# Kernel optimization log

Measured on AMD Instinct MI355X. Metric: run time of the kernel, lower is better.

Reference implementation:

```python
import jax, jax.numpy as jnp
import numpy as np

N, S, E, H = 4, 2048, 1024, 16
D = E // H  # head dim = 64


def setup_inputs() -> dict:
    key = jax.random.key(0)
    ks = jax.random.split(key, 8)
    return {
        "values": jax.random.normal(ks[0], (N, S, E), dtype=jnp.float32),
        "keys": jax.random.normal(ks[1], (N, S, E), dtype=jnp.float32),
        "queries": jax.random.normal(ks[2], (N, S, E), dtype=jnp.float32),
        "mask": jnp.ones((N, 1, 1, S), dtype=jnp.int32),
        "Wv": jax.random.normal(ks[3], (D, D), dtype=jnp.float32) / np.sqrt(D),
        "Wk": jax.random.normal(ks[4], (D, D), dtype=jnp.float32) / np.sqrt(D),
        "Wq": jax.random.normal(ks[5], (D, D), dtype=jnp.float32) / np.sqrt(D),
        "W_out": jax.random.normal(ks[6], (E, E), dtype=jnp.float32) / np.sqrt(E),
        "b_out": jnp.zeros((E,), dtype=jnp.float32),
    }


def reference(values, keys, queries, mask, Wv, Wk, Wq, W_out, b_out):
    n, q_len = queries.shape[0], queries.shape[1]
    v = values.reshape(n, -1, H, D)
    k = keys.reshape(n, -1, H, D)
    q = queries.reshape(n, q_len, H, D)
    # per-head linear projections (torch Linear: x @ W.T), shared across heads
    v = jnp.einsum('nlhd,ed->nlhe', v, Wv)
    k = jnp.einsum('nlhd,ed->nlhe', k, Wk)
    q = jnp.einsum('nqhd,ed->nqhe', q, Wq)
    # full score tensor [n, h, q, k], faithful to the original einsum
    energy = jnp.einsum('nqhd,nkhd->nhqk', q, k)
    energy = jnp.where(mask == 0, jnp.float32(-1e20), energy)
    # NOTE: original scales by sqrt(embed_size), not sqrt(head_dim)
    attention = jax.nn.softmax(energy / jnp.sqrt(jnp.float32(E)), axis=3)
    out = jnp.einsum('nhql,nlhd->nqhd', attention, v).reshape(n, q_len, E)
    out = out @ W_out.T + b_out
    return out
```

## Files before the change

### kernel.cpp

```cpp
#include <hip/hip_runtime.h>
#include <stdint.h>

#define N_B 4
#define SEQ 2048
#define EMB 1024
#define NH  16
#define HD  64
#define NHT 64
#define BQ  128
#define BK  64

typedef __attribute__((ext_vector_type(8))) short bf16x8;
typedef __attribute__((ext_vector_type(4))) float f32x4;
typedef __attribute__((ext_vector_type(2))) unsigned int u32x2;

__device__ __forceinline__ short f2bf(float x) {
  unsigned u = __float_as_uint(x);
  u += 0x7fffu + ((u >> 16) & 1u);
  return (short)(u >> 16);
}

#if __has_builtin(__builtin_amdgcn_cvt_pk_bf16_f32)
typedef __attribute__((ext_vector_type(2))) __bf16 bf16v2;
__device__ __forceinline__ unsigned pkbf(float a, float b) {
  bf16v2 r = __builtin_amdgcn_cvt_pk_bf16_f32(a, b);
  union { bf16v2 v; unsigned u; } c; c.v = r; return c.u;
}
#else
__device__ __forceinline__ unsigned pkbf(float a, float b) {
  return (unsigned)(unsigned short)f2bf(a) | ((unsigned)(unsigned short)f2bf(b) << 16);
}
#endif

__device__ __forceinline__ void swap32p(unsigned a, unsigned b, unsigned& r0, unsigned& r1) {
#if __has_builtin(__builtin_amdgcn_permlane32_swap)
  u32x2 r = __builtin_amdgcn_permlane32_swap(a, b, false, false);
  r0 = r[0]; r1 = r[1];
#else
  unsigned as = (unsigned)__shfl_xor((int)a, 32, 64), bs = (unsigned)__shfl_xor((int)b, 32, 64);
  int lo = (threadIdx.x & 32) == 0;
  r0 = lo ? a : bs;
  r1 = lo ? as : b;
#endif
}
__device__ __forceinline__ void swap16p(unsigned a, unsigned b, unsigned& r0, unsigned& r1) {
#if __has_builtin(__builtin_amdgcn_permlane16_swap)
  u32x2 r = __builtin_amdgcn_permlane16_swap(a, b, false, false);
  r0 = r[0]; r1 = r[1];
#else
  unsigned as = (unsigned)__shfl_xor((int)a, 16, 64), bs = (unsigned)__shfl_xor((int)b, 16, 64);
  int ev = (threadIdx.x & 16) == 0;
  r0 = ev ? a : bs;
  r1 = ev ? as : b;
#endif
}

__device__ __forceinline__ void glds16(const short* g, short* l) {
  __builtin_amdgcn_global_load_lds(
      (const __attribute__((address_space(1))) unsigned int*)g,
      (__attribute__((address_space(3))) unsigned int*)l, 16, 0, 0);
}

__device__ __forceinline__ int swz_src(int lane) {
  return (((lane & 7) ^ ((lane >> 3) & 7)) * 8) + ((lane >> 3) * 64);
}
__device__ __forceinline__ int swz_rd(int r, int k) {
  return r * 64 + ((k ^ (r & 7)) * 8);
}

__global__ __launch_bounds__(256) void projm_kernel(
    const float* __restrict__ Xq, const float* __restrict__ Xk, const float* __restrict__ Xv,
    const float* __restrict__ Wq, const float* __restrict__ Wk, const float* __restrict__ Wv,
    short* __restrict__ Qp, short* __restrict__ Kp, short* __restrict__ Vp,
    const float* __restrict__ Wo, short* __restrict__ Wb) {
  int tid = threadIdx.x;
  int z = blockIdx.z;
  if (z == 3) {
    int flat = blockIdx.x + blockIdx.y * 16;
    int idx = (flat * 256 + tid) * 4;
    f32x4 v = *(const f32x4*)(Wo + idx);
    uint2 u; u.x = pkbf(v.x, v.y); u.y = pkbf(v.z, v.w);
    *(uint2*)(Wb + idx) = u;
    return;
  }
  const float* X = (z == 0) ? Xq : (z == 1) ? Xk : Xv;
  const float* W = (z == 0) ? Wq : (z == 1) ? Wk : Wv;
  short* out = (z == 0) ? Qp : (z == 1) ? Kp : Vp;
  int transposed = (z == 2);
  float oscale = (z == 0) ? 0.04508422f : 1.0f;

  __shared__ __attribute__((aligned(16))) short Xs[128 * 64];
  __shared__ __attribute__((aligned(16))) short Ws[64 * 64];
  int w = tid >> 6, lane = tid & 63;
  int quad = lane >> 4, l15 = lane & 15;
  int sb = blockIdx.x * 128;
  int nh = blockIdx.y;
  int n = nh >> 4, h = nh & 15;
  int r4 = tid >> 2, c0 = (tid & 3) * 16;
  int ch0 = c0 >> 3;
#pragma unroll
  for (int rr = 0; rr < 2; rr++) {
    int row = rr * 64 + r4;
    const float* gp = X + ((size_t)(n * SEQ + sb + row)) * EMB + h * HD + c0;
    f32x4 a = *(const f32x4*)gp, b = *(const f32x4*)(gp + 4);
    f32x4 c = *(const f32x4*)(gp + 8), d = *(const f32x4*)(gp + 12);
    uint4 u0, u1;
    u0.x = pkbf(a.x, a.y); u0.y = pkbf(a.z, a.w);
    u0.z = pkbf(b.x, b.y); u0.w = pkbf(b.z, b.w);
    u1.x = pkbf(c.x, c.y); u1.y = pkbf(c.z, c.w);
    u1.z = pkbf(d.x, d.y); u1.w = pkbf(d.z, d.w);
    *(uint4*)&Xs[row * 64 + ((ch0 ^ (row & 7)) * 8)] = u0;
    *(uint4*)&Xs[row * 64 + (((ch0 + 1) ^ (row & 7)) * 8)] = u1;
  }
  {
    int e = r4;
    const float* wp = W + e * HD + c0;
    f32x4 a = *(const f32x4*)wp, b = *(const f32x4*)(wp + 4);
    f32x4 c = *(const f32x4*)(wp + 8), d = *(const f32x4*)(wp + 12);
    uint4 u0, u1;
    u0.x = pkbf(a.x, a.y); u0.y = pkbf(a.z, a.w);
    u0.z = pkbf(b.x, b.y); u0.w = pkbf(b.z, b.w);
    u1.x = pkbf(c.x, c.y); u1.y = pkbf(c.z, c.w);
    u1.z = pkbf(d.x, d.y); u1.w = pkbf(d.z, d.w);
    *(uint4*)&Ws[e * 64 + ((ch0 ^ (e & 7)) * 8)] = u0;
    *(uint4*)&Ws[e * 64 + (((ch0 + 1) ^ (e & 7)) * 8)] = u1;
  }
  __syncthreads();
  f32x4 acc[2][4] = {};
#pragma unroll
  for (int ch = 0; ch < 2; ch++) {
    bf16x8 af[2], bfr[4];
#pragma unroll
    for (int mi = 0; mi < 2; mi++)
      af[mi] = *(const bf16x8*)&Xs[swz_rd(w * 32 + mi * 16 + l15, ch * 4 + quad)];
#pragma unroll
    for (int ni = 0; ni < 4; ni++)
      bfr[ni] = *(const bf16x8*)&Ws[swz_rd(ni * 16 + l15, ch * 4 + quad)];
#pragma unroll
    for (int mi = 0; mi < 2; mi++)
#pragma unroll
      for (int ni = 0; ni < 4; ni++)
        acc[mi][ni] = __builtin_amdgcn_mfma_f32_16x16x32_bf16(af[mi], bfr[ni], acc[mi][ni], 0, 0, 0);
  }
  if (!transposed) {
#pragma unroll
    for (int mi = 0; mi < 2; mi++)
#pragma unroll
      for (int ni = 0; ni < 4; ni++)
#pragma unroll
        for (int r = 0; r < 4; r++) {
          int s = sb + w * 32 + mi * 16 + quad * 4 + r;
          out[((size_t)nh * SEQ + s) * HD + ni * 16 + l15] = f2bf(acc[mi][ni][r] * oscale);
        }
  } else {
#pragma unroll
    for (int mi = 0; mi < 2; mi++)
#pragma unroll
      for (int ni = 0; ni < 4; ni++) {
        int e2 = ni * 16 + l15;
        int s0 = sb + w * 32 + mi * 16 + quad * 4;
        uint2 u;
        u.x = pkbf(acc[mi][ni][0], acc[mi][ni][1]);
        u.y = pkbf(acc[mi][ni][2], acc[mi][ni][3]);
        *(uint2*)(out + ((size_t)nh * HD + e2) * SEQ + s0) = u;
      }
  }
}

__global__ __launch_bounds__(256, 4) void attn_kernel(
    const short* __restrict__ Qg, const short* __restrict__ Kg,
    const short* __restrict__ Vg, const int* __restrict__ maskp,
    short* __restrict__ AO) {
  __shared__ __attribute__((aligned(16))) short L[16384];

  int tid = threadIdx.x;
  int w = tid >> 6, lane = tid & 63;
  int quad = lane >> 4, l15 = lane & 15;
  int nh = blockIdx.x;
  int qt0 = blockIdx.y * BQ;
  int n = nh >> 4, h = nh & 15;
  int ssrc = swz_src(lane);
  int vrow = lane >> 3;
  int vcg = (((lane & 7) ^ ((lane >> 3) & 7)) * 8);
  const int NT = SEQ / BK;

  const short* kb = Kg + (size_t)nh * SEQ * HD;
  const short* vb = Vg + (size_t)nh * HD * SEQ;

  const short* qbase = Qg + ((size_t)nh * SEQ + qt0) * HD;
#pragma unroll
  for (int i = 0; i < 4; i++) {
    int idx = (w * 4 + i) * 512;
    glds16(qbase + idx + ssrc, &L[8192 + idx]);
  }
#pragma unroll
  for (int i = 0; i < 2; i++) {
    int idx = (w * 2 + i) * 512;
    glds16(kb + idx + ssrc, &L[idx]);
    int d = (w * 2 + i) * 8 + vrow;
    glds16(vb + (size_t)d * SEQ + vcg, &L[4096 + idx]);
  }
  int mcur = maskp[n * SEQ + lane];
  __syncthreads();
  bf16x8 qf[2][2];
#pragma unroll
  for (int nt = 0; nt < 2; nt++)
#pragma unroll
    for (int ch = 0; ch < 2; ch++)
      qf[nt][ch] = *(const bf16x8*)&L[8192 + swz_rd(w * 32 + nt * 16 + l15, ch * 4 + quad)];
  __syncthreads();

  bf16x8 vone;
#pragma unroll
  for (int j = 0; j < 8; j++) vone[j] = (short)0x3F80;

  f32x4 Oacc[2][4] = {};
  f32x4 lacc[2] = {};

  for (int kt = 0; kt < NT; kt++) {
    int cur = kt & 1;
    const short* Kb = &L[cur * 8192];
    const short* Vb = &L[cur * 8192 + 4096];
    if (kt + 1 < NT) {
      size_t k0n = (size_t)(kt + 1) * BK;
      short* Kn = &L[(cur ^ 1) * 8192];
#pragma unroll
      for (int i = 0; i < 2; i++) {
        int idx = (w * 2 + i) * 512;
        glds16(kb + k0n * HD + idx + ssrc, &Kn[idx]);
        int d = (w * 2 + i) * 8 + vrow;
        glds16(vb + (size_t)d * SEQ + k0n + vcg, &Kn[4096 + idx]);
      }
    }
    int knx = (kt + 1 < NT) ? kt + 1 : kt;
    int mnxt = maskp[n * SEQ + knx * BK + lane];

    unsigned long long mb = __ballot(mcur != 0);
    bool anymask = (mb != ~0ull);

#pragma unroll
    for (int half = 0; half < 2; half++) {
      f32x4 st[2][2];
      __builtin_amdgcn_s_setprio(1);
#pragma unroll
      for (int m2 = 0; m2 < 2; m2++) {
        int mt = half * 2 + m2;
        bf16x8 kf0 = *(const bf16x8*)&Kb[swz_rd(mt * 16 + l15, quad)];
        bf16x8 kf1 = *(const bf16x8*)&Kb[swz_rd(mt * 16 + l15, 4 + quad)];
#pragma unroll
        for (int nt = 0; nt < 2; nt++) {
          f32x4 a = {0.f, 0.f, 0.f, 0.f};
          a = __builtin_amdgcn_mfma_f32_16x16x32_bf16(kf0, qf[nt][0], a, 0, 0, 0);
          a = __builtin_amdgcn_mfma_f32_16x16x32_bf16(kf1, qf[nt][1], a, 0, 0, 0);
          st[m2][nt] = a;
        }
      }
      __builtin_amdgcn_s_setprio(0);
      if (anymask) {
#pragma unroll
        for (int m2 = 0; m2 < 2; m2++)
#pragma unroll
          for (int r = 0; r < 4; r++) {
            int kk = (half * 2 + m2) * 16 + quad * 4 + r;
            if (!((mb >> kk) & 1)) { st[m2][0][r] = -1e20f; st[m2][1][r] = -1e20f; }
          }
      }
      bf16x8 pf[2];
#pragma unroll
      for (int nt = 0; nt < 2; nt++) {
        unsigned A0 = pkbf(__builtin_amdgcn_exp2f(st[0][nt][0]), __builtin_amdgcn_exp2f(st[0][nt][1]));
        unsigned A1 = pkbf(__builtin_amdgcn_exp2f(st[0][nt][2]), __builtin_amdgcn_exp2f(st[0][nt][3]));
        unsigned B0 = pkbf(__builtin_amdgcn_exp2f(st[1][nt][0]), __builtin_amdgcn_exp2f(st[1][nt][1]));
        unsigned B1 = pkbf(__builtin_amdgcn_exp2f(st[1][nt][2]), __builtin_amdgcn_exp2f(st[1][nt][3]));
        unsigned r0, r1, s0, s1, o0, o1, o2, o3;
        swap32p(A0, B0, r0, r1);
        swap16p(r0, r1, o0, o2);
        swap32p(A1, B1, s0, s1);
        swap16p(s0, s1, o1, o3);
        union { unsigned u[4]; bf16x8 v; } c;
        c.u[0] = o0; c.u[1] = o1; c.u[2] = o2; c.u[3] = o3;
        pf[nt] = c.v;
      }

      __builtin_amdgcn_s_setprio(1);
#pragma unroll
      for (int qt = 0; qt < 2; qt++)
        lacc[qt] = __builtin_amdgcn_mfma_f32_16x16x32_bf16(pf[qt], vone, lacc[qt], 0, 0, 0);
#pragma unroll
      for (int dt = 0; dt < 4; dt++) {
        bf16x8 vf = *(const bf16x8*)&Vb[swz_rd(dt * 16 + l15, half * 4 + quad)];
#pragma unroll
        for (int qt = 0; qt < 2; qt++)
          Oacc[qt][dt] = __builtin_amdgcn_mfma_f32_16x16x32_bf16(pf[qt], vf, Oacc[qt][dt], 0, 0, 0);
      }
      __builtin_amdgcn_s_setprio(0);
    }
    mcur = mnxt;
    __syncthreads();
  }
#pragma unroll
  for (int qt = 0; qt < 2; qt++)
#pragma unroll
    for (int r = 0; r < 4; r++) {
      float inv = 1.0f / lacc[qt][r];
      int qrow = qt0 + w * 32 + qt * 16 + quad * 4 + r;
      size_t rowb = ((size_t)n * SEQ + qrow) * EMB + h * HD;
#pragma unroll
      for (int dt = 0; dt < 4; dt++)
        AO[rowb + dt * 16 + l15] = f2bf(Oacc[qt][dt][r] * inv);
    }
}

__global__ __launch_bounds__(256, 2) void gemm_kernel(const short* __restrict__ A,
                                                      const short* __restrict__ B,
                                                      const float* __restrict__ bias,
                                                      float* __restrict__ C) {
  __shared__ __attribute__((aligned(16))) short As[2][128 * 64];
  __shared__ __attribute__((aligned(16))) short Bs[2][128 * 64];
  int tid = threadIdx.x;
  int w = tid >> 6, lane = tid & 63;
  int quad = lane >> 4, l15 = lane & 15;
  int m0 = blockIdx.x * 128, n0 = blockIdx.y * 128;
  int mw = (w & 1) * 64, nw = (w >> 1) * 64;
  int lrow = lane >> 3;
  int lcg = ((lane & 7) ^ ((lane >> 3) & 7)) * 8;
  f32x4 acc[4][4] = {};
#pragma unroll
  for (int i = 0; i < 4; i++) {
    int ii = w * 4 + i;
    int r = ii * 8 + lrow;
    glds16(A + (size_t)(m0 + r) * 1024 + lcg, &As[0][ii * 512]);
    glds16(B + (size_t)(n0 + r) * 1024 + lcg, &Bs[0][ii * 512]);
  }
  __syncthreads();
  for (int kt = 0; kt < 16; kt++) {
    int cur = kt & 1;
    if (kt < 15) {
      int k0n = (kt + 1) * 64;
#pragma unroll
      for (int i = 0; i < 4; i++) {
        int ii = w * 4 + i;
        int r = ii * 8 + lrow;
        glds16(A + (size_t)(m0 + r) * 1024 + k0n + lcg, &As[cur ^ 1][ii * 512]);
        glds16(B + (size_t)(n0 + r) * 1024 + k0n + lcg, &Bs[cur ^ 1][ii * 512]);
      }
    }
#pragma unroll
    for (int ch = 0; ch < 2; ch++) {
      bf16x8 af[4], bfr[4];
#pragma unroll
      for (int mi = 0; mi < 4; mi++)
        af[mi] = *(const bf16x8*)&As[cur][swz_rd(mw + mi * 16 + l15, ch * 4 + quad)];
#pragma unroll
      for (int ni = 0; ni < 4; ni++)
        bfr[ni] = *(const bf16x8*)&Bs[cur][swz_rd(nw + ni * 16 + l15, ch * 4 + quad)];
#pragma unroll
      for (int mi = 0; mi < 4; mi++)
#pragma unroll
        for (int ni = 0; ni < 4; ni++)
          acc[mi][ni] = __builtin_amdgcn_mfma_f32_16x16x32_bf16(af[mi], bfr[ni], acc[mi][ni], 0, 0, 0);
    }
    __syncthreads();
  }
#pragma unroll
  for (int ni = 0; ni < 4; ni++) {
    int col = n0 + nw + ni * 16 + l15;
    float bv = bias[col];
#pragma unroll
    for (int mi = 0; mi < 4; mi++) {
      int rb = m0 + mw + mi * 16 + quad * 4;
#pragma unroll
      for (int r = 0; r < 4; r++)
        C[(size_t)(rb + r) * 1024 + col] = acc[mi][ni][r] + bv;
    }
  }
}

extern "C" void kernel_launch(void* const* d_in, const int* in_sizes, int n_in,
                              void* d_out, int out_size, void* d_ws, size_t ws_size,
                              hipStream_t stream) {
  const float* values  = (const float*)d_in[0];
  const float* keys    = (const float*)d_in[1];
  const float* queries = (const float*)d_in[2];
  const int*   mask    = (const int*)d_in[3];
  const float* Wv = (const float*)d_in[4];
  const float* Wk = (const float*)d_in[5];
  const float* Wq = (const float*)d_in[6];
  const float* Wo = (const float*)d_in[7];
  const float* bo = (const float*)d_in[8];
  float* out = (float*)d_out;

  short* ws = (short*)d_ws;
  short* Qp = ws;
  short* Kp = Qp + (size_t)NHT * SEQ * HD;
  short* Vp = Kp + (size_t)NHT * SEQ * HD;
  short* AO = Vp + (size_t)NHT * SEQ * HD;
  short* Wb = AO + (size_t)N_B * SEQ * EMB;

  dim3 pg(SEQ / 128, NHT, 4);
  projm_kernel<<<pg, dim3(256), 0, stream>>>(queries, keys, values, Wq, Wk, Wv,
                                             Qp, Kp, Vp, Wo, Wb);
  dim3 ag(NHT, SEQ / BQ);
  attn_kernel<<<ag, dim3(256), 0, stream>>>(Qp, Kp, Vp, mask, AO);
  dim3 gg(8192 / 128, 1024 / 128);
  gemm_kernel<<<gg, dim3(256), 0, stream>>>(AO, Wb, bo, out);
}
```

Before: 265.4 us.

## Enlarge attention query tile to 256 with 8 warps and two-tile K/V stages

Raises the attention block to 512 threads covering 256 query rows, so each K/V tile staged in LDS is reused by twice as many warps. K/V staging now processes two 64-key tiles per barrier, double-buffered across 64KB of LDS, which halves the number of __syncthreads per sequence. Q fragments are loaded straight from global into registers instead of going through LDS. The cost is a larger LDS footprint and fewer blocks (512 in total on 256 CUs), which can lower occupancy and leave load imbalance.

```diff
diff --git a/kernel.cpp b/kernel.cpp
--- a/kernel.cpp
+++ b/kernel.cpp
@@ -7,7 +7,7 @@
 #define NH  16
 #define HD  64
 #define NHT 64
-#define BQ  128
+#define BQ  256
 #define BK  64
 
 typedef __attribute__((ext_vector_type(8))) short bf16x8;
@@ -167,11 +167,11 @@
   }
 }
 
-__global__ __launch_bounds__(256, 4) void attn_kernel(
+__global__ __launch_bounds__(512, 4) void attn_kernel(
     const short* __restrict__ Qg, const short* __restrict__ Kg,
     const short* __restrict__ Vg, const int* __restrict__ maskp,
     short* __restrict__ AO) {
-  __shared__ __attribute__((aligned(16))) short L[16384];
+  __shared__ __attribute__((aligned(16))) short L[32768];
 
   int tid = threadIdx.x;
   int w = tid >> 6, lane = tid & 63;
@@ -182,32 +182,31 @@
   int ssrc = swz_src(lane);
   int vrow = lane >> 3;
   int vcg = (((lane & 7) ^ ((lane >> 3) & 7)) * 8);
-  const int NT = SEQ / BK;
+  const int NS = SEQ / (2 * BK);
 
   const short* kb = Kg + (size_t)nh * SEQ * HD;
   const short* vb = Vg + (size_t)nh * HD * SEQ;
 
-  const short* qbase = Qg + ((size_t)nh * SEQ + qt0) * HD;
-#pragma unroll
-  for (int i = 0; i < 4; i++) {
-    int idx = (w * 4 + i) * 512;
-    glds16(qbase + idx + ssrc, &L[8192 + idx]);
-  }
-#pragma unroll
-  for (int i = 0; i < 2; i++) {
-    int idx = (w * 2 + i) * 512;
-    glds16(kb + idx + ssrc, &L[idx]);
-    int d = (w * 2 + i) * 8 + vrow;
-    glds16(vb + (size_t)d * SEQ + vcg, &L[4096 + idx]);
-  }
-  int mcur = maskp[n * SEQ + lane];
-  __syncthreads();
   bf16x8 qf[2][2];
-#pragma unroll
-  for (int nt = 0; nt < 2; nt++)
-#pragma unroll
-    for (int ch = 0; ch < 2; ch++)
-      qf[nt][ch] = *(const bf16x8*)&L[8192 + swz_rd(w * 32 + nt * 16 + l15, ch * 4 + quad)];
+  {
+    const short* qb = Qg + ((size_t)nh * SEQ + qt0 + w * 32) * HD;
+#pragma unroll
+    for (int nt = 0; nt < 2; nt++)
+#pragma unroll
+      for (int ch = 0; ch < 2; ch++)
+        qf[nt][ch] = *(const bf16x8*)(qb + (nt * 16 + l15) * HD + ch * 32 + quad * 8);
+  }
+
+  auto stage_tile = [&](int t, int base) {
+    glds16(kb + (size_t)t * (BK * HD) + w * 512 + ssrc, &L[base + w * 512]);
+    int d = w * 8 + vrow;
+    glds16(vb + (size_t)d * SEQ + t * BK + vcg, &L[base + 4096 + w * 512]);
+  };
+
+  stage_tile(0, 0);
+  stage_tile(1, 8192);
+  int mA = maskp[n * SEQ + lane];
+  int mB = maskp[n * SEQ + BK + lane];
   __syncthreads();
 
   bf16x8 vone;
@@ -217,85 +216,84 @@
   f32x4 Oacc[2][4] = {};
   f32x4 lacc[2] = {};
 
-  for (int kt = 0; kt < NT; kt++) {
-    int cur = kt & 1;
-    const short* Kb = &L[cur * 8192];
-    const short* Vb = &L[cur * 8192 + 4096];
-    if (kt + 1 < NT) {
-      size_t k0n = (size_t)(kt + 1) * BK;
-      short* Kn = &L[(cur ^ 1) * 8192];
-#pragma unroll
-      for (int i = 0; i < 2; i++) {
-        int idx = (w * 2 + i) * 512;
-        glds16(kb + k0n * HD + idx + ssrc, &Kn[idx]);
-        int d = (w * 2 + i) * 8 + vrow;
-        glds16(vb + (size_t)d * SEQ + k0n + vcg, &Kn[4096 + idx]);
+  for (int s = 0; s < NS; s++) {
+    int p = s & 1;
+    if (s + 1 < NS) {
+      int t0 = 2 * s + 2;
+      stage_tile(t0, (p ^ 1) * 16384);
+      stage_tile(t0 + 1, (p ^ 1) * 16384 + 8192);
+    }
+    int tn = (s + 1 < NS) ? (2 * s + 2) : 0;
+    int mAn = maskp[n * SEQ + tn * BK + lane];
+    int mBn = maskp[n * SEQ + (tn + 1) * BK + lane];
+
+#pragma unroll
+    for (int j = 0; j < 2; j++) {
+      const short* Kb = &L[p * 16384 + j * 8192];
+      const short* Vb = Kb + 4096;
+      unsigned long long mb = __ballot((j == 0 ? mA : mB) != 0);
+      bool anymask = (mb != ~0ull);
+
+#pragma unroll
+      for (int half = 0; half < 2; half++) {
+        f32x4 st[2][2];
+        __builtin_amdgcn_s_setprio(1);
+#pragma unroll
+        for (int m2 = 0; m2 < 2; m2++) {
+          int mt = half * 2 + m2;
+          bf16x8 kf0 = *(const bf16x8*)&Kb[swz_rd(mt * 16 + l15, quad)];
+          bf16x8 kf1 = *(const bf16x8*)&Kb[swz_rd(mt * 16 + l15, 4 + quad)];
+#pragma unroll
+          for (int nt = 0; nt < 2; nt++) {
+            f32x4 a = {0.f, 0.f, 0.f, 0.f};
+            a = __builtin_amdgcn_mfma_f32_16x16x32_bf16(kf0, qf[nt][0], a, 0, 0, 0);
+            a = __builtin_amdgcn_mfma_f32_16x16x32_bf16(kf1, qf[nt][1], a, 0, 0, 0);
+            st[m2][nt] = a;
+          }
+        }
+        __builtin_amdgcn_s_setprio(0);
+        if (anymask) {
+#pragma unroll
+          for (int m2 = 0; m2 < 2; m2++)
+#pragma unroll
+            for (int r = 0; r < 4; r++) {
+              int kk = (half * 2 + m2) * 16 + quad * 4 + r;
+              if (!((mb >> kk) & 1)) { st[m2][0][r] = -1e20f; st[m2][1][r] = -1e20f; }
+            }
+        }
+        bf16x8 pf[2];
+#pragma unroll
+        for (int nt = 0; nt < 2; nt++) {
+          unsigned A0 = pkbf(__builtin_amdgcn_exp2f(st[0][nt][0]), __builtin_amdgcn_exp2f(st[0][nt][1]));
+          unsigned A1 = pkbf(__builtin_amdgcn_exp2f(st[0][nt][2]), __builtin_amdgcn_exp2f(st[0][nt][3]));
+          unsigned B0 = pkbf(__builtin_amdgcn_exp2f(st[1][nt][0]), __builtin_amdgcn_exp2f(st[1][nt][1]));
+          unsigned B1 = pkbf(__builtin_amdgcn_exp2f(st[1][nt][2]), __builtin_amdgcn_exp2f(st[1][nt][3]));
+          unsigned r0, r1, s0, s1, o0, o1, o2, o3;
+          swap32p(A0, B0, r0, r1);
+          swap16p(r0, r1, o0, o2);
+          swap32p(A1, B1, s0, s1);
+          swap16p(s0, s1, o1, o3);
+          union { unsigned u[4]; bf16x8 v; } c;
+          c.u[0] = o0; c.u[1] = o1; c.u[2] = o2; c.u[3] = o3;
+          pf[nt] = c.v;
+        }
+
+        __builtin_amdgcn_s_setprio(1);
+#pragma unroll
+        for (int qt = 0; qt < 2; qt++)
+          lacc[qt] = __builtin_amdgcn_mfma_f32_16x16x32_bf16(pf[qt], vone, lacc[qt], 0, 0, 0);
+#pragma unroll
+        for (int dt = 0; dt < 4; dt++) {
+          bf16x8 vf = *(const bf16x8*)&Vb[swz_rd(dt * 16 + l15, half * 4 + quad)];
+#pragma unroll
+          for (int qt = 0; qt < 2; qt++)
+            Oacc[qt][dt] = __builtin_amdgcn_mfma_f32_16x16x32_bf16(pf[qt], vf, Oacc[qt][dt], 0, 0, 0);
+        }
+        __builtin_amdgcn_s_setprio(0);
       }
     }
-    int knx = (kt + 1 < NT) ? kt + 1 : kt;
-    int mnxt = maskp[n * SEQ + knx * BK + lane];
-
-    unsigned long long mb = __ballot(mcur != 0);
-    bool anymask = (mb != ~0ull);
-
-#pragma unroll
-    for (int half = 0; half < 2; half++) {
-      f32x4 st[2][2];
-      __builtin_amdgcn_s_setprio(1);
-#pragma unroll
-      for (int m2 = 0; m2 < 2; m2++) {
-        int mt = half * 2 + m2;
-        bf16x8 kf0 = *(const bf16x8*)&Kb[swz_rd(mt * 16 + l15, quad)];
-        bf16x8 kf1 = *(const bf16x8*)&Kb[swz_rd(mt * 16 + l15, 4 + quad)];
-#pragma unroll
-        for (int nt = 0; nt < 2; nt++) {
-          f32x4 a = {0.f, 0.f, 0.f, 0.f};
-          a = __builtin_amdgcn_mfma_f32_16x16x32_bf16(kf0, qf[nt][0], a, 0, 0, 0);
-          a = __builtin_amdgcn_mfma_f32_16x16x32_bf16(kf1, qf[nt][1], a, 0, 0, 0);
-          st[m2][nt] = a;
-        }
-      }
-      __builtin_amdgcn_s_setprio(0);
-      if (anymask) {
-#pragma unroll
-        for (int m2 = 0; m2 < 2; m2++)
-#pragma unroll
-          for (int r = 0; r < 4; r++) {
-            int kk = (half * 2 + m2) * 16 + quad * 4 + r;
-            if (!((mb >> kk) & 1)) { st[m2][0][r] = -1e20f; st[m2][1][r] = -1e20f; }
-          }
-      }
-      bf16x8 pf[2];
-#pragma unroll
-      for (int nt = 0; nt < 2; nt++) {
-        unsigned A0 = pkbf(__builtin_amdgcn_exp2f(st[0][nt][0]), __builtin_amdgcn_exp2f(st[0][nt][1]));
-        unsigned A1 = pkbf(__builtin_amdgcn_exp2f(st[0][nt][2]), __builtin_amdgcn_exp2f(st[0][nt][3]));
-        unsigned B0 = pkbf(__builtin_amdgcn_exp2f(st[1][nt][0]), __builtin_amdgcn_exp2f(st[1][nt][1]));
-        unsigned B1 = pkbf(__builtin_amdgcn_exp2f(st[1][nt][2]), __builtin_amdgcn_exp2f(st[1][nt][3]));
-        unsigned r0, r1, s0, s1, o0, o1, o2, o3;
-        swap32p(A0, B0, r0, r1);
-        swap16p(r0, r1, o0, o2);
-        swap32p(A1, B1, s0, s1);
-        swap16p(s0, s1, o1, o3);
-        union { unsigned u[4]; bf16x8 v; } c;
-        c.u[0] = o0; c.u[1] = o1; c.u[2] = o2; c.u[3] = o3;
-        pf[nt] = c.v;
-      }
-
-      __builtin_amdgcn_s_setprio(1);
-#pragma unroll
-      for (int qt = 0; qt < 2; qt++)
-        lacc[qt] = __builtin_amdgcn_mfma_f32_16x16x32_bf16(pf[qt], vone, lacc[qt], 0, 0, 0);
-#pragma unroll
-      for (int dt = 0; dt < 4; dt++) {
-        bf16x8 vf = *(const bf16x8*)&Vb[swz_rd(dt * 16 + l15, half * 4 + quad)];
-#pragma unroll
-        for (int qt = 0; qt < 2; qt++)
-          Oacc[qt][dt] = __builtin_amdgcn_mfma_f32_16x16x32_bf16(pf[qt], vf, Oacc[qt][dt], 0, 0, 0);
-      }
-      __builtin_amdgcn_s_setprio(0);
-    }
-    mcur = mnxt;
+    mA = mAn;
+    mB = mBn;
     __syncthreads();
   }
 #pragma unroll
@@ -401,7 +399,7 @@
   projm_kernel<<<pg, dim3(256), 0, stream>>>(queries, keys, values, Wq, Wk, Wv,
                                              Qp, Kp, Vp, Wo, Wb);
   dim3 ag(NHT, SEQ / BQ);
-  attn_kernel<<<ag, dim3(256), 0, stream>>>(Qp, Kp, Vp, mask, AO);
+  attn_kernel<<<ag, dim3(512), 0, stream>>>(Qp, Kp, Vp, mask, AO);
   dim3 gg(8192 / 128, 1024 / 128);
   gemm_kernel<<<gg, dim3(256), 0, stream>>>(AO, Wb, bo, out);
 }
```

Result: no change. 267.7 us (+0.9%).
